# Performance work log

Measured on AMD Instinct MI355X. Metric: run time of the kernel, lower is better.

The kernel has to match this reference:

```python
import jax, jax.numpy as jnp
import numpy as np

# ---- problem constants (match init_kwargs) ----
LAM = 1.0; MU = 1.0; D0 = 1.0; NMIN = 1.0; NMAX = 99; ALPHA = 2.0
BATCH = 2048; N_STEPS = 64; T = 1.0; HIDDEN = 128


def _U(x):
    return D0 / (x + NMIN) ** ALPHA


def _delta_n(pre_n, dt, forward, k, rng):
    # faithful numpy port of PolymerDiffusion.delta_N (jump sizes shared across batch per call)
    log_res = -np.log(rng.random(k))
    lsk = np.concatenate([[0.0], np.cumsum(log_res / LAM / 2)])
    msk = np.concatenate([[0.0], np.cumsum(log_res / MU / 2)])
    jl = int(np.searchsorted(lsk[1:], dt, side='right'))  # first j with dt < lsk[j+1]
    jm = int(np.searchsorted(msk[1:], dt, side='right'))
    if jl >= k: jl = 0  # no break -> delta stays 0
    if jm >= k: jm = 0
    eta = rng.random(pre_n.shape[0])
    if forward:
        d_up = np.where(pre_n <= NMAX - jl, jl, 0)
        d_dn = np.where(pre_n >= jm, -jm, 0)
    else:
        d_up = np.where(pre_n >= jl, jl, 0)
        d_dn = np.where(pre_n <= NMAX - jm, -jm, 0)
    return np.where(eta < 0.5, d_up, d_dn).astype(np.float64)


def _get_samples(dt, N, rng):
    B = BATCH
    X1 = np.zeros((B, N + 1)); X1[:, 0] = rng.integers(0, NMAX + 1, B)
    X2 = np.zeros((B, N + 1))
    dB = rng.standard_normal((B, N)) * np.sqrt(dt)
    for i in range(N):
        X1[:, i + 1] = X1[:, i] + _delta_n(X1[:, i], dt, True, 5, rng)
        X2[:, i + 1] = X2[:, i] + _U(X1[:, i]) * dt + dB[:, i]
    X1b = rng.integers(0, NMAX + 1, (B, N + 1)).astype(np.float64)
    X2b = np.zeros((B, N + 1))
    dBb = rng.standard_normal((B, N)) * np.sqrt(dt)
    X1b[:, N] = X1[:, N]; X2b[:, N] = X2[:, N]
    for i in range(N):
        X1b[:, N - i - 1] = X1b[:, N - i] - _delta_n(X1b[:, N - i], dt, False, 5, rng)
        X2b[:, N - i - 1] = X2b[:, N - i] - _U(X1b[:, N - i]) * dt - dBb[:, N - i - 1]
    return (np.concatenate([X1, X1b], 0), np.concatenate([X2, X2b], 0), np.concatenate([dB, dBb], 0))


def setup_inputs() -> dict:
    rng = np.random.default_rng(0)
    dt = T / N_STEPS
    n_np, s_np, dB_np = _get_samples(dt, N_STEPS, rng)
    key = jax.random.key(0)
    ks = jax.random.split(key, 4)
    def w(k, fi, fo):
        return jax.random.normal(k, (fi, fo), jnp.float32) / np.sqrt(fi).astype(np.float32)
    return {
        'W1': w(ks[0], 2, HIDDEN), 'b1': jnp.zeros(HIDDEN, jnp.float32),
        'W2': w(ks[1], HIDDEN, HIDDEN), 'b2': jnp.zeros(HIDDEN, jnp.float32),
        'W3': w(ks[2], HIDDEN, HIDDEN), 'b3': jnp.zeros(HIDDEN, jnp.float32),
        'W4': w(ks[3], HIDDEN, NMAX + 1), 'b4': jnp.zeros(NMAX + 1, jnp.float32),
        'samples_n': jnp.asarray(n_np, jnp.int32),      # [2B, N+1]
        'samples_s': jnp.asarray(s_np, jnp.float32),    # [2B, N+1]
        'samples_deltaB': jnp.asarray(dB_np, jnp.float32),  # [2B, N]
        't': jnp.float32(T),
    }


def reference(W1, b1, W2, b2, W3, b3, W4, b4, samples_n, samples_s, samples_deltaB, t):
    N = samples_deltaB.shape[1]
    dt = t / N
    out_dim = W4.shape[1]  # nmax + 1

    def u_scalar(s, tk, n):
        x = jnp.stack([s, tk])  # [2]
        h = jnp.tanh(x @ W1 + b1)
        h = jnp.tanh(h @ W2 + b2)
        h = jnp.tanh(h @ W3 + b3)
        return (h @ W4 + b4)[n]

    du = jax.grad(u_scalar, 0)
    ddu = jax.grad(du, 0)
    u_v = jax.vmap(u_scalar)
    du_v = jax.vmap(du)
    ddu_v = jax.vmap(ddu)

    B2 = samples_s.shape[0]
    tk0 = jnp.broadcast_to(t, (B2,))
    sN, nN = samples_s[:, N], samples_n[:, N]
    u = u_v(sN, tk0, nN)
    ps = du_v(sN, tk0, nN)
    pss = ddu_v(sN, tk0, nN)

    # step i uses column N-1-i and time tk = t - i*dt (tk decremented AFTER get_partial, as in source)
    dB_rev = samples_deltaB[:, ::-1].T            # [N, 2B]
    s_rev = samples_s[:, N - 1::-1].T             # [N, 2B]
    n_rev = samples_n[:, N - 1::-1].T             # [N, 2B]
    tks = t - dt * jnp.arange(N, dtype=samples_s.dtype)  # [N]

    def step(carry, xs):
        u, ps, pss = carry
        dB, s_col, n_col, tk = xs
        u = u - ps * dB - pss * dt * 0.5
        tkv = jnp.broadcast_to(tk, s_col.shape)
        ps = du_v(s_col, tkv, n_col)
        pss = ddu_v(s_col, tkv, n_col)
        return (u, ps, pss), None

    (u, _, _), _ = jax.lax.scan(step, (u, ps, pss), (dB_rev, s_rev, n_rev, tks))

    beta = 1e6
    s0 = samples_s[:, 0]
    u0 = jnp.sqrt(beta / (2 * jnp.pi)) * jnp.exp(-beta * s0 ** 2 / 2) / out_dim
    return (u[:, None], u0[:, None])
```

## Files before the change

kernel.cpp:

```cpp
#include <hip/hip_runtime.h>
#include <hip/hip_fp16.h>
#include <math.h>

#define HIDDEN 128
#define NSTEP  64
#define BATCH2 4096
#define OUTD   100

typedef __attribute__((ext_vector_type(8))) _Float16 f16x8;
typedef __attribute__((ext_vector_type(4))) float    f32x4;

static __device__ __forceinline__ f32x4 mfma32(f16x8 a, f16x8 b, f32x4 c) {
    return __builtin_amdgcn_mfma_f32_16x16x32_f16(a, b, c, 0, 0, 0);
}
static __device__ __forceinline__ unsigned h2u(__half2 h) {
    return __builtin_bit_cast(unsigned, h);
}
static __device__ __forceinline__ __half2 u2h(unsigned u) {
    return __builtin_bit_cast(__half2, u);
}
static __device__ __forceinline__ f16x8 frag8(__half2 a, __half2 b, __half2 c, __half2 d) {
    uint4 p = { h2u(a), h2u(b), h2u(c), h2u(d) };
    return __builtin_bit_cast(f16x8, p);
}
static __device__ __forceinline__ f16x8 catu2(uint2 lo, uint2 hi) {
    uint4 p = { lo.x, lo.y, hi.x, hi.y };
    return __builtin_bit_cast(f16x8, p);
}

static __device__ __forceinline__ void load_lds16(const void* g, void* l) {
    __builtin_amdgcn_global_load_lds(
        (const __attribute__((address_space(1))) void*)g,
        (__attribute__((address_space(3))) void*)l, 16, 0, 0);
}

static __device__ __forceinline__ void tanh_chain_h2(
    __half2 z, __half2 zd, __half2 zdd,
    __half2& a, __half2& ad, __half2& add)
{
    const __half2 one = __float2half2_rn(1.0f);
    const __half2 two = __float2half2_rn(2.0f);
    __half2 e = h2exp(__hadd2(z, z));
    __half2 w = __hmul2(two, h2rcp(__hadd2(e, one)));
    a  = __hsub2(one, w);
    __half2 g = __hmul2(w, __hsub2(two, w));
    ad = __hmul2(g, zd);
    __half2 p = __hmul2(a, zd);
    __half2 u = __hadd2(p, p);
    add = __hsub2(__hmul2(g, zdd), __hmul2(u, ad));
}

__global__ __launch_bounds__(256) void setup_kernel(
    const float* __restrict__ W2, const float* __restrict__ W3,
    const float* __restrict__ W4,
    const float* __restrict__ b2, const float* __restrict__ b3,
    const float* __restrict__ samples_s,
    __half* __restrict__ wbf, float* __restrict__ out)
{
    int t = blockIdx.x * blockDim.x + threadIdx.x;
    {
        int l = t >> 14;
        int f = t & 16383;
        int row = f >> 7;
        int m   = f & 127;
        float v = (l ? W3 : W2)[f];
        int c, q, i;
        if (l == 0) {
            c = row >> 5; q = (row >> 3) & 3; i = row & 7;
        } else {
            c = row >> 5;
            int rem = row & 31;
            q = (rem >> 2) & 3;
            i = ((rem >> 4) << 2) | (rem & 3);
        }
        int pos = (l << 14) + ((((m >> 4) << 2) + c) << 9)
                + ((16 * q + (m & 15)) << 3) + i;
        wbf[pos] = __float2half(v);
    }
    if (t < OUTD * HIDDEN) {
        int h = t / OUTD, n = t - h * OUTD;
        wbf[32768 + n * HIDDEN + h] = __float2half(W4[t]);
    }
    if (t < 256) {
        const float* bp = (t < 128) ? b2 : b3;
        wbf[45568 + t] = __float2half(bp[t & 127]);
    }
    if (t < BATCH2) {
        out[t] = 0.0f;
        float s0 = samples_s[t * (NSTEP + 1)];
        out[BATCH2 + t] = 3.9894228040143267f * expf(-500000.0f * s0 * s0);
    }
}

__global__ __launch_bounds__(256, 4) void eval_kernel(
    const float* __restrict__ W1, const float* __restrict__ b1,
    const float* __restrict__ b4,
    const __half* __restrict__ wbf,
    const int*   __restrict__ samples_n,
    const float* __restrict__ samples_s,
    const float* __restrict__ samples_dB,
    const float* __restrict__ tptr,
    float* __restrict__ out)
{
    __shared__ __align__(16) short  ldsW[HIDDEN * HIDDEN];
    __shared__ __align__(16) __half ldsB[256];

    const int tid  = threadIdx.x;
    const int w    = tid >> 6;
    const int lane = tid & 63;
    const int m16  = lane & 15;
    const int q    = lane >> 4;
    const int b    = blockIdx.x;

    {
        const short* g2 = (const short*)wbf;
        #pragma unroll
        for (int it = 0; it < 8; ++it) {
            int idx = w * 8 + it;
            load_lds16(g2 + idx * 512 + lane * 8, ldsW + idx * 512);
        }
    }
    if (tid < 128) {
        ((unsigned*)ldsB)[tid] = ((const unsigned*)(wbf + 45568))[tid];
    }

    const float t  = tptr[0];
    const float dt = t / (float)NSTEP;
    const int   j  = 16 * w + m16;
    const int   c  = NSTEP - j;
    const float s  = samples_s[b * (NSTEP + 1) + c];
    const int   n  = samples_n[b * (NSTEP + 1) + c];
    const float dB = samples_dB[b * NSTEP + (NSTEP - 1 - j)];
    const float tk = (j == 0) ? t : t - dt * (float)(j - 1);

    f16x8 B1v[4], B1d[4], B1dd[4];
    const __half2 zero2 = __float2half2_rn(0.0f);
    #pragma unroll
    for (int ck = 0; ck < 4; ++ck) {
        const int h0 = 32 * ck + 8 * q;
        float4 wa0 = *(const float4*)(W1 + h0);
        float4 wa1 = *(const float4*)(W1 + h0 + 4);
        float4 wb0 = *(const float4*)(W1 + HIDDEN + h0);
        float4 wb1 = *(const float4*)(W1 + HIDDEN + h0 + 4);
        float4 bb0 = *(const float4*)(b1 + h0);
        float4 bb1 = *(const float4*)(b1 + h0 + 4);
        __half2 a[4], ad[4], add[4];
        {
            __half2 z  = __floats2half2_rn(fmaf(wa0.x, s, fmaf(wb0.x, tk, bb0.x)),
                                           fmaf(wa0.y, s, fmaf(wb0.y, tk, bb0.y)));
            tanh_chain_h2(z, __floats2half2_rn(wa0.x, wa0.y), zero2, a[0], ad[0], add[0]);
            z  = __floats2half2_rn(fmaf(wa0.z, s, fmaf(wb0.z, tk, bb0.z)),
                                   fmaf(wa0.w, s, fmaf(wb0.w, tk, bb0.w)));
            tanh_chain_h2(z, __floats2half2_rn(wa0.z, wa0.w), zero2, a[1], ad[1], add[1]);
            z  = __floats2half2_rn(fmaf(wa1.x, s, fmaf(wb1.x, tk, bb1.x)),
                                   fmaf(wa1.y, s, fmaf(wb1.y, tk, bb1.y)));
            tanh_chain_h2(z, __floats2half2_rn(wa1.x, wa1.y), zero2, a[2], ad[2], add[2]);
            z  = __floats2half2_rn(fmaf(wa1.z, s, fmaf(wb1.z, tk, bb1.z)),
                                   fmaf(wa1.w, s, fmaf(wb1.w, tk, bb1.w)));
            tanh_chain_h2(z, __floats2half2_rn(wa1.z, wa1.w), zero2, a[3], ad[3], add[3]);
        }
        B1v[ck]  = frag8(a[0],  a[1],  a[2],  a[3]);
        B1d[ck]  = frag8(ad[0], ad[1], ad[2], ad[3]);
        B1dd[ck] = frag8(add[0], add[1], add[2], add[3]);
    }

    __syncthreads();

    uint2 Nv[8], Nd[8], Ndd[8];
    #pragma unroll
    for (int mt = 0; mt < 8; ++mt) {
        f32x4 aV = {0.f,0.f,0.f,0.f}, aD = {0.f,0.f,0.f,0.f}, aDD = {0.f,0.f,0.f,0.f};
        #pragma unroll
        for (int ck = 0; ck < 4; ++ck) {
            f16x8 aw = *(const f16x8*)(ldsW + ((mt * 4 + ck) << 9) + (lane << 3));
            aV  = mfma32(aw, B1v[ck],  aV );
            aD  = mfma32(aw, B1d[ck],  aD );
            aDD = mfma32(aw, B1dd[ck], aDD);
        }
        uint2 bh = *(const uint2*)(ldsB + 16 * mt + 4 * q);
        __half2 z0 = __hadd2(__floats2half2_rn(aV[0], aV[1]), u2h(bh.x));
        __half2 z1 = __hadd2(__floats2half2_rn(aV[2], aV[3]), u2h(bh.y));
        __half2 a0, ad0, add0, a1, ad1, add1;
        tanh_chain_h2(z0, __floats2half2_rn(aD[0], aD[1]),
                      __floats2half2_rn(aDD[0], aDD[1]), a0, ad0, add0);
        tanh_chain_h2(z1, __floats2half2_rn(aD[2], aD[3]),
                      __floats2half2_rn(aDD[2], aDD[3]), a1, ad1, add1);
        Nv[mt]  = (uint2){ h2u(a0),  h2u(a1)  };
        Nd[mt]  = (uint2){ h2u(ad0), h2u(ad1) };
        Ndd[mt] = (uint2){ h2u(add0), h2u(add1) };
    }

    __syncthreads();

    {
        const short* g3 = (const short*)(wbf + HIDDEN * HIDDEN);
        #pragma unroll
        for (int it = 0; it < 8; ++it) {
            int idx = w * 8 + it;
            load_lds16(g3 + idx * 512 + lane * 8, ldsW + idx * 512);
        }
    }

    f16x8 B2v[4], B2d[4], B2dd[4];
    #pragma unroll
    for (int ck = 0; ck < 4; ++ck) {
        B2v[ck]  = catu2(Nv[2*ck],  Nv[2*ck+1]);
        B2d[ck]  = catu2(Nd[2*ck],  Nd[2*ck+1]);
        B2dd[ck] = catu2(Ndd[2*ck], Ndd[2*ck+1]);
    }
    __syncthreads();

    const __half* __restrict__ w4t = wbf + 2 * HIDDEN * HIDDEN;
    __half2 accV = zero2, accD = zero2, accDD = zero2;
    #pragma unroll
    for (int mt = 0; mt < 8; ++mt) {
        f32x4 aV = {0.f,0.f,0.f,0.f}, aD = {0.f,0.f,0.f,0.f}, aDD = {0.f,0.f,0.f,0.f};
        #pragma unroll
        for (int ck = 0; ck < 4; ++ck) {
            f16x8 aw = *(const f16x8*)(ldsW + ((mt * 4 + ck) << 9) + (lane << 3));
            aV  = mfma32(aw, B2v[ck],  aV );
            aD  = mfma32(aw, B2d[ck],  aD );
            aDD = mfma32(aw, B2dd[ck], aDD);
        }
        const int h0 = 16 * mt + 4 * q;
        uint2 w4u = *(const uint2*)(w4t + n * HIDDEN + h0);
        __half2 w4lo = u2h(w4u.x), w4hi = u2h(w4u.y);
        uint2 bh = *(const uint2*)(ldsB + 128 + h0);
        __half2 z0 = __hadd2(__floats2half2_rn(aV[0], aV[1]), u2h(bh.x));
        __half2 z1 = __hadd2(__floats2half2_rn(aV[2], aV[3]), u2h(bh.y));
        __half2 a0, ad0, add0, a1, ad1, add1;
        tanh_chain_h2(z0, __floats2half2_rn(aD[0], aD[1]),
                      __floats2half2_rn(aDD[0], aDD[1]), a0, ad0, add0);
        tanh_chain_h2(z1, __floats2half2_rn(aD[2], aD[3]),
                      __floats2half2_rn(aDD[2], aDD[3]), a1, ad1, add1);
        accV  = __hfma2(a0,  w4lo, accV );  accV  = __hfma2(a1,  w4hi, accV );
        accD  = __hfma2(ad0, w4lo, accD );  accD  = __hfma2(ad1, w4hi, accD );
        accDD = __hfma2(add0, w4lo, accDD); accDD = __hfma2(add1, w4hi, accDD);
    }
    float sv  = __low2float(accV)  + __high2float(accV);
    float sd  = __low2float(accD)  + __high2float(accD);
    float sdd = __low2float(accDD) + __high2float(accDD);

    sd  += __shfl_xor(sd,  16, 64);  sd  += __shfl_xor(sd,  32, 64);
    sdd += __shfl_xor(sdd, 16, 64);  sdd += __shfl_xor(sdd, 32, 64);
    sv  += __shfl_xor(sv,  16, 64);  sv  += __shfl_xor(sv,  32, 64);

    float contrib = -(sd * dB + sdd * dt * 0.5f);
    if (j == 0) contrib += sv + b4[n];

    contrib += __shfl_xor(contrib, 1, 64);
    contrib += __shfl_xor(contrib, 2, 64);
    contrib += __shfl_xor(contrib, 4, 64);
    contrib += __shfl_xor(contrib, 8, 64);
    if (lane == 0) atomicAdd(&out[b], contrib);
}

extern "C" void kernel_launch(void* const* d_in, const int* in_sizes, int n_in,
                              void* d_out, int out_size, void* d_ws, size_t ws_size,
                              hipStream_t stream) {
    const float* W1 = (const float*)d_in[0];
    const float* b1 = (const float*)d_in[1];
    const float* W2 = (const float*)d_in[2];
    const float* b2 = (const float*)d_in[3];
    const float* W3 = (const float*)d_in[4];
    const float* b3 = (const float*)d_in[5];
    const float* W4 = (const float*)d_in[6];
    const float* b4 = (const float*)d_in[7];
    const int*   sn  = (const int*)d_in[8];
    const float* ss  = (const float*)d_in[9];
    const float* sdB = (const float*)d_in[10];
    const float* t   = (const float*)d_in[11];
    float* out = (float*)d_out;
    __half* wbf = (__half*)d_ws;

    setup_kernel<<<(2 * HIDDEN * HIDDEN) / 256, 256, 0, stream>>>(
        W2, W3, W4, b2, b3, ss, wbf, out);
    eval_kernel<<<BATCH2, 256, 0, stream>>>(
        W1, b1, b4, wbf, sn, ss, sdB, t, out);
}
```

Baseline: 148.6 us.

## Process two batch samples per block to amortize LDS weight loads

Each eval block now handles two batch rows, so the W2/W3 weight tiles staged into LDS are reused across two samples and half as many blocks run. The per-block partial sums are combined through a small LDS buffer and written directly, replacing the atomicAdd. Output zeroing and the u0 computation move from the setup kernel into the eval kernel. Register pressure roughly doubles for activation fragments, so the occupancy hint drops from 4 to 3 waves per SIMD, which risks lower latency hiding.

```diff
diff --git a/kernel.cpp b/kernel.cpp
--- a/kernel.cpp
+++ b/kernel.cpp
@@ -54,8 +54,7 @@
     const float* __restrict__ W2, const float* __restrict__ W3,
     const float* __restrict__ W4,
     const float* __restrict__ b2, const float* __restrict__ b3,
-    const float* __restrict__ samples_s,
-    __half* __restrict__ wbf, float* __restrict__ out)
+    __half* __restrict__ wbf)
 {
     int t = blockIdx.x * blockDim.x + threadIdx.x;
     {
@@ -85,14 +84,9 @@
         const float* bp = (t < 128) ? b2 : b3;
         wbf[45568 + t] = __float2half(bp[t & 127]);
     }
-    if (t < BATCH2) {
-        out[t] = 0.0f;
-        float s0 = samples_s[t * (NSTEP + 1)];
-        out[BATCH2 + t] = 3.9894228040143267f * expf(-500000.0f * s0 * s0);
-    }
-}
-
-__global__ __launch_bounds__(256, 4) void eval_kernel(
+}
+
+__global__ __launch_bounds__(256, 3) void eval_kernel(
     const float* __restrict__ W1, const float* __restrict__ b1,
     const float* __restrict__ b4,
     const __half* __restrict__ wbf,
@@ -104,13 +98,14 @@
 {
     __shared__ __align__(16) short  ldsW[HIDDEN * HIDDEN];
     __shared__ __align__(16) __half ldsB[256];
+    __shared__ float ldsR[2][4];
 
     const int tid  = threadIdx.x;
     const int w    = tid >> 6;
     const int lane = tid & 63;
     const int m16  = lane & 15;
     const int q    = lane >> 4;
-    const int b    = blockIdx.x;
+    const int b0   = blockIdx.x * 2;
 
     {
         const short* g2 = (const short*)wbf;
@@ -128,12 +123,17 @@
     const float dt = t / (float)NSTEP;
     const int   j  = 16 * w + m16;
     const int   c  = NSTEP - j;
-    const float s  = samples_s[b * (NSTEP + 1) + c];
-    const int   n  = samples_n[b * (NSTEP + 1) + c];
-    const float dB = samples_dB[b * NSTEP + (NSTEP - 1 - j)];
     const float tk = (j == 0) ? t : t - dt * (float)(j - 1);
-
-    f16x8 B1v[4], B1d[4], B1dd[4];
+    float sS[2]; int nn[2]; float dBs[2];
+    #pragma unroll
+    for (int p = 0; p < 2; ++p) {
+        int bb = b0 + p;
+        sS[p]  = samples_s[bb * (NSTEP + 1) + c];
+        nn[p]  = samples_n[bb * (NSTEP + 1) + c];
+        dBs[p] = samples_dB[bb * NSTEP + (NSTEP - 1 - j)];
+    }
+
+    f16x8 B1v[2][4], B1d[2][4], B1dd[2][4];
     const __half2 zero2 = __float2half2_rn(0.0f);
     #pragma unroll
     for (int ck = 0; ck < 4; ++ck) {
@@ -144,50 +144,55 @@
         float4 wb1 = *(const float4*)(W1 + HIDDEN + h0 + 4);
         float4 bb0 = *(const float4*)(b1 + h0);
         float4 bb1 = *(const float4*)(b1 + h0 + 4);
-        __half2 a[4], ad[4], add[4];
-        {
-            __half2 z  = __floats2half2_rn(fmaf(wa0.x, s, fmaf(wb0.x, tk, bb0.x)),
-                                           fmaf(wa0.y, s, fmaf(wb0.y, tk, bb0.y)));
+        #pragma unroll
+        for (int p = 0; p < 2; ++p) {
+            float s = sS[p];
+            __half2 a[4], ad[4], add[4];
+            __half2 z = __floats2half2_rn(fmaf(wa0.x, s, fmaf(wb0.x, tk, bb0.x)),
+                                          fmaf(wa0.y, s, fmaf(wb0.y, tk, bb0.y)));
             tanh_chain_h2(z, __floats2half2_rn(wa0.x, wa0.y), zero2, a[0], ad[0], add[0]);
-            z  = __floats2half2_rn(fmaf(wa0.z, s, fmaf(wb0.z, tk, bb0.z)),
-                                   fmaf(wa0.w, s, fmaf(wb0.w, tk, bb0.w)));
+            z = __floats2half2_rn(fmaf(wa0.z, s, fmaf(wb0.z, tk, bb0.z)),
+                                  fmaf(wa0.w, s, fmaf(wb0.w, tk, bb0.w)));
             tanh_chain_h2(z, __floats2half2_rn(wa0.z, wa0.w), zero2, a[1], ad[1], add[1]);
-            z  = __floats2half2_rn(fmaf(wa1.x, s, fmaf(wb1.x, tk, bb1.x)),
-                                   fmaf(wa1.y, s, fmaf(wb1.y, tk, bb1.y)));
+            z = __floats2half2_rn(fmaf(wa1.x, s, fmaf(wb1.x, tk, bb1.x)),
+                                  fmaf(wa1.y, s, fmaf(wb1.y, tk, bb1.y)));
             tanh_chain_h2(z, __floats2half2_rn(wa1.x, wa1.y), zero2, a[2], ad[2], add[2]);
-            z  = __floats2half2_rn(fmaf(wa1.z, s, fmaf(wb1.z, tk, bb1.z)),
-                                   fmaf(wa1.w, s, fmaf(wb1.w, tk, bb1.w)));
+            z = __floats2half2_rn(fmaf(wa1.z, s, fmaf(wb1.z, tk, bb1.z)),
+                                  fmaf(wa1.w, s, fmaf(wb1.w, tk, bb1.w)));
             tanh_chain_h2(z, __floats2half2_rn(wa1.z, wa1.w), zero2, a[3], ad[3], add[3]);
-        }
-        B1v[ck]  = frag8(a[0],  a[1],  a[2],  a[3]);
-        B1d[ck]  = frag8(ad[0], ad[1], ad[2], ad[3]);
-        B1dd[ck] = frag8(add[0], add[1], add[2], add[3]);
-    }
-
-    __syncthreads();
-
-    uint2 Nv[8], Nd[8], Ndd[8];
-    #pragma unroll
-    for (int mt = 0; mt < 8; ++mt) {
-        f32x4 aV = {0.f,0.f,0.f,0.f}, aD = {0.f,0.f,0.f,0.f}, aDD = {0.f,0.f,0.f,0.f};
-        #pragma unroll
-        for (int ck = 0; ck < 4; ++ck) {
-            f16x8 aw = *(const f16x8*)(ldsW + ((mt * 4 + ck) << 9) + (lane << 3));
-            aV  = mfma32(aw, B1v[ck],  aV );
-            aD  = mfma32(aw, B1d[ck],  aD );
-            aDD = mfma32(aw, B1dd[ck], aDD);
-        }
-        uint2 bh = *(const uint2*)(ldsB + 16 * mt + 4 * q);
-        __half2 z0 = __hadd2(__floats2half2_rn(aV[0], aV[1]), u2h(bh.x));
-        __half2 z1 = __hadd2(__floats2half2_rn(aV[2], aV[3]), u2h(bh.y));
-        __half2 a0, ad0, add0, a1, ad1, add1;
-        tanh_chain_h2(z0, __floats2half2_rn(aD[0], aD[1]),
-                      __floats2half2_rn(aDD[0], aDD[1]), a0, ad0, add0);
-        tanh_chain_h2(z1, __floats2half2_rn(aD[2], aD[3]),
-                      __floats2half2_rn(aDD[2], aDD[3]), a1, ad1, add1);
-        Nv[mt]  = (uint2){ h2u(a0),  h2u(a1)  };
-        Nd[mt]  = (uint2){ h2u(ad0), h2u(ad1) };
-        Ndd[mt] = (uint2){ h2u(add0), h2u(add1) };
+            B1v[p][ck]  = frag8(a[0],  a[1],  a[2],  a[3]);
+            B1d[p][ck]  = frag8(ad[0], ad[1], ad[2], ad[3]);
+            B1dd[p][ck] = frag8(add[0], add[1], add[2], add[3]);
+        }
+    }
+
+    __syncthreads();
+
+    uint2 Nv[2][8], Nd[2][8], Ndd[2][8];
+    #pragma unroll
+    for (int p = 0; p < 2; ++p) {
+        #pragma unroll
+        for (int mt = 0; mt < 8; ++mt) {
+            f32x4 aV = {0.f,0.f,0.f,0.f}, aD = {0.f,0.f,0.f,0.f}, aDD = {0.f,0.f,0.f,0.f};
+            #pragma unroll
+            for (int ck = 0; ck < 4; ++ck) {
+                f16x8 aw = *(const f16x8*)(ldsW + ((mt * 4 + ck) << 9) + (lane << 3));
+                aV  = mfma32(aw, B1v[p][ck],  aV );
+                aD  = mfma32(aw, B1d[p][ck],  aD );
+                aDD = mfma32(aw, B1dd[p][ck], aDD);
+            }
+            uint2 bh = *(const uint2*)(ldsB + 16 * mt + 4 * q);
+            __half2 z0 = __hadd2(__floats2half2_rn(aV[0], aV[1]), u2h(bh.x));
+            __half2 z1 = __hadd2(__floats2half2_rn(aV[2], aV[3]), u2h(bh.y));
+            __half2 a0, ad0, add0, a1, ad1, add1;
+            tanh_chain_h2(z0, __floats2half2_rn(aD[0], aD[1]),
+                          __floats2half2_rn(aDD[0], aDD[1]), a0, ad0, add0);
+            tanh_chain_h2(z1, __floats2half2_rn(aD[2], aD[3]),
+                          __floats2half2_rn(aDD[2], aDD[3]), a1, ad1, add1);
+            Nv[p][mt]  = (uint2){ h2u(a0),  h2u(a1)  };
+            Nd[p][mt]  = (uint2){ h2u(ad0), h2u(ad1) };
+            Ndd[p][mt] = (uint2){ h2u(add0), h2u(add1) };
+        }
     }
 
     __syncthreads();
@@ -200,59 +205,64 @@
             load_lds16(g3 + idx * 512 + lane * 8, ldsW + idx * 512);
         }
     }
-
-    f16x8 B2v[4], B2d[4], B2dd[4];
-    #pragma unroll
-    for (int ck = 0; ck < 4; ++ck) {
-        B2v[ck]  = catu2(Nv[2*ck],  Nv[2*ck+1]);
-        B2d[ck]  = catu2(Nd[2*ck],  Nd[2*ck+1]);
-        B2dd[ck] = catu2(Ndd[2*ck], Ndd[2*ck+1]);
-    }
     __syncthreads();
 
     const __half* __restrict__ w4t = wbf + 2 * HIDDEN * HIDDEN;
-    __half2 accV = zero2, accD = zero2, accDD = zero2;
-    #pragma unroll
-    for (int mt = 0; mt < 8; ++mt) {
-        f32x4 aV = {0.f,0.f,0.f,0.f}, aD = {0.f,0.f,0.f,0.f}, aDD = {0.f,0.f,0.f,0.f};
-        #pragma unroll
-        for (int ck = 0; ck < 4; ++ck) {
-            f16x8 aw = *(const f16x8*)(ldsW + ((mt * 4 + ck) << 9) + (lane << 3));
-            aV  = mfma32(aw, B2v[ck],  aV );
-            aD  = mfma32(aw, B2d[ck],  aD );
-            aDD = mfma32(aw, B2dd[ck], aDD);
-        }
-        const int h0 = 16 * mt + 4 * q;
-        uint2 w4u = *(const uint2*)(w4t + n * HIDDEN + h0);
-        __half2 w4lo = u2h(w4u.x), w4hi = u2h(w4u.y);
-        uint2 bh = *(const uint2*)(ldsB + 128 + h0);
-        __half2 z0 = __hadd2(__floats2half2_rn(aV[0], aV[1]), u2h(bh.x));
-        __half2 z1 = __hadd2(__floats2half2_rn(aV[2], aV[3]), u2h(bh.y));
-        __half2 a0, ad0, add0, a1, ad1, add1;
-        tanh_chain_h2(z0, __floats2half2_rn(aD[0], aD[1]),
-                      __floats2half2_rn(aDD[0], aDD[1]), a0, ad0, add0);
-        tanh_chain_h2(z1, __floats2half2_rn(aD[2], aD[3]),
-                      __floats2half2_rn(aDD[2], aDD[3]), a1, ad1, add1);
-        accV  = __hfma2(a0,  w4lo, accV );  accV  = __hfma2(a1,  w4hi, accV );
-        accD  = __hfma2(ad0, w4lo, accD );  accD  = __hfma2(ad1, w4hi, accD );
-        accDD = __hfma2(add0, w4lo, accDD); accDD = __hfma2(add1, w4hi, accDD);
-    }
-    float sv  = __low2float(accV)  + __high2float(accV);
-    float sd  = __low2float(accD)  + __high2float(accD);
-    float sdd = __low2float(accDD) + __high2float(accDD);
-
-    sd  += __shfl_xor(sd,  16, 64);  sd  += __shfl_xor(sd,  32, 64);
-    sdd += __shfl_xor(sdd, 16, 64);  sdd += __shfl_xor(sdd, 32, 64);
-    sv  += __shfl_xor(sv,  16, 64);  sv  += __shfl_xor(sv,  32, 64);
-
-    float contrib = -(sd * dB + sdd * dt * 0.5f);
-    if (j == 0) contrib += sv + b4[n];
-
-    contrib += __shfl_xor(contrib, 1, 64);
-    contrib += __shfl_xor(contrib, 2, 64);
-    contrib += __shfl_xor(contrib, 4, 64);
-    contrib += __shfl_xor(contrib, 8, 64);
-    if (lane == 0) atomicAdd(&out[b], contrib);
+    float contrib[2];
+    #pragma unroll
+    for (int p = 0; p < 2; ++p) {
+        __half2 accV = zero2, accD = zero2, accDD = zero2;
+        #pragma unroll
+        for (int mt = 0; mt < 8; ++mt) {
+            f32x4 aV = {0.f,0.f,0.f,0.f}, aD = {0.f,0.f,0.f,0.f}, aDD = {0.f,0.f,0.f,0.f};
+            #pragma unroll
+            for (int ck = 0; ck < 4; ++ck) {
+                f16x8 aw = *(const f16x8*)(ldsW + ((mt * 4 + ck) << 9) + (lane << 3));
+                aV  = mfma32(aw, catu2(Nv[p][2*ck],  Nv[p][2*ck+1]),  aV );
+                aD  = mfma32(aw, catu2(Nd[p][2*ck],  Nd[p][2*ck+1]),  aD );
+                aDD = mfma32(aw, catu2(Ndd[p][2*ck], Ndd[p][2*ck+1]), aDD);
+            }
+            const int h0 = 16 * mt + 4 * q;
+            uint2 w4u = *(const uint2*)(w4t + nn[p] * HIDDEN + h0);
+            __half2 w4lo = u2h(w4u.x), w4hi = u2h(w4u.y);
+            uint2 bh = *(const uint2*)(ldsB + 128 + h0);
+            __half2 z0 = __hadd2(__floats2half2_rn(aV[0], aV[1]), u2h(bh.x));
+            __half2 z1 = __hadd2(__floats2half2_rn(aV[2], aV[3]), u2h(bh.y));
+            __half2 a0, ad0, add0, a1, ad1, add1;
+            tanh_chain_h2(z0, __floats2half2_rn(aD[0], aD[1]),
+                          __floats2half2_rn(aDD[0], aDD[1]), a0, ad0, add0);
+            tanh_chain_h2(z1, __floats2half2_rn(aD[2], aD[3]),
+                          __floats2half2_rn(aDD[2], aDD[3]), a1, ad1, add1);
+            accV  = __hfma2(a0,  w4lo, accV );  accV  = __hfma2(a1,  w4hi, accV );
+            accD  = __hfma2(ad0, w4lo, accD );  accD  = __hfma2(ad1, w4hi, accD );
+            accDD = __hfma2(add0, w4lo, accDD); accDD = __hfma2(add1, w4hi, accDD);
+        }
+        float sv  = __low2float(accV)  + __high2float(accV);
+        float sd  = __low2float(accD)  + __high2float(accD);
+        float sdd = __low2float(accDD) + __high2float(accDD);
+        sd  += __shfl_xor(sd,  16, 64);  sd  += __shfl_xor(sd,  32, 64);
+        sdd += __shfl_xor(sdd, 16, 64);  sdd += __shfl_xor(sdd, 32, 64);
+        sv  += __shfl_xor(sv,  16, 64);  sv  += __shfl_xor(sv,  32, 64);
+        float cb = -(sd * dBs[p] + sdd * dt * 0.5f);
+        if (j == 0) cb += sv + b4[nn[p]];
+        cb += __shfl_xor(cb, 1, 64);
+        cb += __shfl_xor(cb, 2, 64);
+        cb += __shfl_xor(cb, 4, 64);
+        cb += __shfl_xor(cb, 8, 64);
+        contrib[p] = cb;
+    }
+    if (lane == 0) {
+        ldsR[0][w] = contrib[0];
+        ldsR[1][w] = contrib[1];
+    }
+    __syncthreads();
+
+    if (tid < 2) {
+        float u = ldsR[tid][0] + ldsR[tid][1] + ldsR[tid][2] + ldsR[tid][3];
+        out[b0 + tid] = u;
+        float s0 = samples_s[(b0 + tid) * (NSTEP + 1)];
+        out[BATCH2 + b0 + tid] = 3.9894228040143267f * expf(-500000.0f * s0 * s0);
+    }
 }
 
 extern "C" void kernel_launch(void* const* d_in, const int* in_sizes, int n_in,
@@ -274,7 +284,7 @@
     __half* wbf = (__half*)d_ws;
 
     setup_kernel<<<(2 * HIDDEN * HIDDEN) / 256, 256, 0, stream>>>(
-        W2, W3, W4, b2, b3, ss, wbf, out);
-    eval_kernel<<<BATCH2, 256, 0, stream>>>(
+        W2, W3, W4, b2, b3, wbf);
+    eval_kernel<<<BATCH2 / 2, 256, 0, stream>>>(
         W1, b1, b4, wbf, sn, ss, sdB, t, out);
 }
```

Result: slower. 243.0 us (+63.6%).

## Read MLP weights straight from global memory instead of staging in LDS

Applied to the files above, without the earlier changes.

Removes the 32 KB LDS staging of W2/W3 and biases, along with the three block barriers, and has each wave load its MFMA A-fragments directly from global memory (L1/L2 cached). Dropping LDS use can raise occupancy and removes the synchronisation points. The cost is repeated global/L2 traffic for the same weights across waves and blocks, with load latency now exposed at each MFMA. It also limits the value-accumulator work to wave 0.

```diff
diff --git a/kernel.cpp b/kernel.cpp
--- a/kernel.cpp
+++ b/kernel.cpp
@@ -26,12 +26,6 @@
 static __device__ __forceinline__ f16x8 catu2(uint2 lo, uint2 hi) {
     uint4 p = { lo.x, lo.y, hi.x, hi.y };
     return __builtin_bit_cast(f16x8, p);
-}
-
-static __device__ __forceinline__ void load_lds16(const void* g, void* l) {
-    __builtin_amdgcn_global_load_lds(
-        (const __attribute__((address_space(1))) void*)g,
-        (__attribute__((address_space(3))) void*)l, 16, 0, 0);
 }
 
 static __device__ __forceinline__ void tanh_chain_h2(
@@ -102,27 +96,12 @@
     const float* __restrict__ tptr,
     float* __restrict__ out)
 {
-    __shared__ __align__(16) short  ldsW[HIDDEN * HIDDEN];
-    __shared__ __align__(16) __half ldsB[256];
-
     const int tid  = threadIdx.x;
     const int w    = tid >> 6;
     const int lane = tid & 63;
     const int m16  = lane & 15;
     const int q    = lane >> 4;
     const int b    = blockIdx.x;
-
-    {
-        const short* g2 = (const short*)wbf;
-        #pragma unroll
-        for (int it = 0; it < 8; ++it) {
-            int idx = w * 8 + it;
-            load_lds16(g2 + idx * 512 + lane * 8, ldsW + idx * 512);
-        }
-    }
-    if (tid < 128) {
-        ((unsigned*)ldsB)[tid] = ((const unsigned*)(wbf + 45568))[tid];
-    }
 
     const float t  = tptr[0];
     const float dt = t / (float)NSTEP;
@@ -132,6 +111,10 @@
     const int   n  = samples_n[b * (NSTEP + 1) + c];
     const float dB = samples_dB[b * NSTEP + (NSTEP - 1 - j)];
     const float tk = (j == 0) ? t : t - dt * (float)(j - 1);
+
+    const short* gW2 = (const short*)wbf + (lane << 3);
+    const short* gW3 = (const short*)(wbf + HIDDEN * HIDDEN) + (lane << 3);
+    const __half* bia = wbf + 45568;
 
     f16x8 B1v[4], B1d[4], B1dd[4];
     const __half2 zero2 = __float2half2_rn(0.0f);
@@ -164,20 +147,18 @@
         B1dd[ck] = frag8(add[0], add[1], add[2], add[3]);
     }
 
-    __syncthreads();
-
     uint2 Nv[8], Nd[8], Ndd[8];
     #pragma unroll
     for (int mt = 0; mt < 8; ++mt) {
         f32x4 aV = {0.f,0.f,0.f,0.f}, aD = {0.f,0.f,0.f,0.f}, aDD = {0.f,0.f,0.f,0.f};
         #pragma unroll
         for (int ck = 0; ck < 4; ++ck) {
-            f16x8 aw = *(const f16x8*)(ldsW + ((mt * 4 + ck) << 9) + (lane << 3));
+            f16x8 aw = *(const f16x8*)(gW2 + ((mt * 4 + ck) << 9));
             aV  = mfma32(aw, B1v[ck],  aV );
             aD  = mfma32(aw, B1d[ck],  aD );
             aDD = mfma32(aw, B1dd[ck], aDD);
         }
-        uint2 bh = *(const uint2*)(ldsB + 16 * mt + 4 * q);
+        uint2 bh = *(const uint2*)(bia + 16 * mt + 4 * q);
         __half2 z0 = __hadd2(__floats2half2_rn(aV[0], aV[1]), u2h(bh.x));
         __half2 z1 = __hadd2(__floats2half2_rn(aV[2], aV[3]), u2h(bh.y));
         __half2 a0, ad0, add0, a1, ad1, add1;
@@ -190,26 +171,6 @@
         Ndd[mt] = (uint2){ h2u(add0), h2u(add1) };
     }
 
-    __syncthreads();
-
-    {
-        const short* g3 = (const short*)(wbf + HIDDEN * HIDDEN);
-        #pragma unroll
-        for (int it = 0; it < 8; ++it) {
-            int idx = w * 8 + it;
-            load_lds16(g3 + idx * 512 + lane * 8, ldsW + idx * 512);
-        }
-    }
-
-    f16x8 B2v[4], B2d[4], B2dd[4];
-    #pragma unroll
-    for (int ck = 0; ck < 4; ++ck) {
-        B2v[ck]  = catu2(Nv[2*ck],  Nv[2*ck+1]);
-        B2d[ck]  = catu2(Nd[2*ck],  Nd[2*ck+1]);
-        B2dd[ck] = catu2(Ndd[2*ck], Ndd[2*ck+1]);
-    }
-    __syncthreads();
-
     const __half* __restrict__ w4t = wbf + 2 * HIDDEN * HIDDEN;
     __half2 accV = zero2, accD = zero2, accDD = zero2;
     #pragma unroll
@@ -217,15 +178,15 @@
         f32x4 aV = {0.f,0.f,0.f,0.f}, aD = {0.f,0.f,0.f,0.f}, aDD = {0.f,0.f,0.f,0.f};
         #pragma unroll
         for (int ck = 0; ck < 4; ++ck) {
-            f16x8 aw = *(const f16x8*)(ldsW + ((mt * 4 + ck) << 9) + (lane << 3));
-            aV  = mfma32(aw, B2v[ck],  aV );
-            aD  = mfma32(aw, B2d[ck],  aD );
-            aDD = mfma32(aw, B2dd[ck], aDD);
+            f16x8 aw = *(const f16x8*)(gW3 + ((mt * 4 + ck) << 9));
+            aV  = mfma32(aw, catu2(Nv[2*ck],  Nv[2*ck+1]),  aV );
+            aD  = mfma32(aw, catu2(Nd[2*ck],  Nd[2*ck+1]),  aD );
+            aDD = mfma32(aw, catu2(Ndd[2*ck], Ndd[2*ck+1]), aDD);
         }
         const int h0 = 16 * mt + 4 * q;
         uint2 w4u = *(const uint2*)(w4t + n * HIDDEN + h0);
         __half2 w4lo = u2h(w4u.x), w4hi = u2h(w4u.y);
-        uint2 bh = *(const uint2*)(ldsB + 128 + h0);
+        uint2 bh = *(const uint2*)(bia + 128 + h0);
         __half2 z0 = __hadd2(__floats2half2_rn(aV[0], aV[1]), u2h(bh.x));
         __half2 z1 = __hadd2(__floats2half2_rn(aV[2], aV[3]), u2h(bh.y));
         __half2 a0, ad0, add0, a1, ad1, add1;
@@ -233,20 +194,24 @@
                       __floats2half2_rn(aDD[0], aDD[1]), a0, ad0, add0);
         tanh_chain_h2(z1, __floats2half2_rn(aD[2], aD[3]),
                       __floats2half2_rn(aDD[2], aDD[3]), a1, ad1, add1);
-        accV  = __hfma2(a0,  w4lo, accV );  accV  = __hfma2(a1,  w4hi, accV );
         accD  = __hfma2(ad0, w4lo, accD );  accD  = __hfma2(ad1, w4hi, accD );
         accDD = __hfma2(add0, w4lo, accDD); accDD = __hfma2(add1, w4hi, accDD);
-    }
-    float sv  = __low2float(accV)  + __high2float(accV);
+        if (w == 0) {
+            accV = __hfma2(a0, w4lo, accV);  accV = __hfma2(a1, w4hi, accV);
+        }
+    }
     float sd  = __low2float(accD)  + __high2float(accD);
     float sdd = __low2float(accDD) + __high2float(accDD);
 
     sd  += __shfl_xor(sd,  16, 64);  sd  += __shfl_xor(sd,  32, 64);
     sdd += __shfl_xor(sdd, 16, 64);  sdd += __shfl_xor(sdd, 32, 64);
-    sv  += __shfl_xor(sv,  16, 64);  sv  += __shfl_xor(sv,  32, 64);
 
     float contrib = -(sd * dB + sdd * dt * 0.5f);
-    if (j == 0) contrib += sv + b4[n];
+    if (w == 0) {
+        float sv = __low2float(accV) + __high2float(accV);
+        sv += __shfl_xor(sv, 16, 64);  sv += __shfl_xor(sv, 32, 64);
+        if (j == 0) contrib += sv + b4[n];
+    }
 
     contrib += __shfl_xor(contrib, 1, 64);
     contrib += __shfl_xor(contrib, 2, 64);
```

Result: slower. 154.4 us (+3.9%).

## Process two samples per block and replace atomics with an LDS reduction

Applied to the files above, without the earlier changes.

Each 512-thread block now handles two batch samples, so every staged W2/W3 tile in LDS is shared by twice the work and each wave loads half as many chunks. The per-sample atomicAdd is replaced by an LDS reduction followed by a plain store. The output zeroing and u0 computation move from the setup kernel into the eval kernel. The value-path accumulation now runs only in the wave that needs it, and the B-fragment concatenation is inlined into the MFMA loop to relieve register pressure. In exchange, launch bounds of 512 threads and 8 blocks may limit registers and occupancy.

```diff
diff --git a/kernel.cpp b/kernel.cpp
--- a/kernel.cpp
+++ b/kernel.cpp
@@ -54,8 +54,7 @@
     const float* __restrict__ W2, const float* __restrict__ W3,
     const float* __restrict__ W4,
     const float* __restrict__ b2, const float* __restrict__ b3,
-    const float* __restrict__ samples_s,
-    __half* __restrict__ wbf, float* __restrict__ out)
+    __half* __restrict__ wbf)
 {
     int t = blockIdx.x * blockDim.x + threadIdx.x;
     {
@@ -85,14 +84,9 @@
         const float* bp = (t < 128) ? b2 : b3;
         wbf[45568 + t] = __float2half(bp[t & 127]);
     }
-    if (t < BATCH2) {
-        out[t] = 0.0f;
-        float s0 = samples_s[t * (NSTEP + 1)];
-        out[BATCH2 + t] = 3.9894228040143267f * expf(-500000.0f * s0 * s0);
-    }
-}
-
-__global__ __launch_bounds__(256, 4) void eval_kernel(
+}
+
+__global__ __launch_bounds__(512, 8) void eval_kernel(
     const float* __restrict__ W1, const float* __restrict__ b1,
     const float* __restrict__ b4,
     const __half* __restrict__ wbf,
@@ -104,19 +98,22 @@
 {
     __shared__ __align__(16) short  ldsW[HIDDEN * HIDDEN];
     __shared__ __align__(16) __half ldsB[256];
+    __shared__ float ldsR[2][4];
 
     const int tid  = threadIdx.x;
     const int w    = tid >> 6;
+    const int p    = w >> 2;
+    const int jw   = w & 3;
     const int lane = tid & 63;
     const int m16  = lane & 15;
     const int q    = lane >> 4;
-    const int b    = blockIdx.x;
+    const int b    = blockIdx.x * 2 + p;
 
     {
         const short* g2 = (const short*)wbf;
         #pragma unroll
-        for (int it = 0; it < 8; ++it) {
-            int idx = w * 8 + it;
+        for (int it = 0; it < 4; ++it) {
+            int idx = w * 4 + it;
             load_lds16(g2 + idx * 512 + lane * 8, ldsW + idx * 512);
         }
     }
@@ -126,7 +123,7 @@
 
     const float t  = tptr[0];
     const float dt = t / (float)NSTEP;
-    const int   j  = 16 * w + m16;
+    const int   j  = 16 * jw + m16;
     const int   c  = NSTEP - j;
     const float s  = samples_s[b * (NSTEP + 1) + c];
     const int   n  = samples_n[b * (NSTEP + 1) + c];
@@ -195,18 +192,10 @@
     {
         const short* g3 = (const short*)(wbf + HIDDEN * HIDDEN);
         #pragma unroll
-        for (int it = 0; it < 8; ++it) {
-            int idx = w * 8 + it;
+        for (int it = 0; it < 4; ++it) {
+            int idx = w * 4 + it;
             load_lds16(g3 + idx * 512 + lane * 8, ldsW + idx * 512);
         }
-    }
-
-    f16x8 B2v[4], B2d[4], B2dd[4];
-    #pragma unroll
-    for (int ck = 0; ck < 4; ++ck) {
-        B2v[ck]  = catu2(Nv[2*ck],  Nv[2*ck+1]);
-        B2d[ck]  = catu2(Nd[2*ck],  Nd[2*ck+1]);
-        B2dd[ck] = catu2(Ndd[2*ck], Ndd[2*ck+1]);
     }
     __syncthreads();
 
@@ -218,9 +207,9 @@
         #pragma unroll
         for (int ck = 0; ck < 4; ++ck) {
             f16x8 aw = *(const f16x8*)(ldsW + ((mt * 4 + ck) << 9) + (lane << 3));
-            aV  = mfma32(aw, B2v[ck],  aV );
-            aD  = mfma32(aw, B2d[ck],  aD );
-            aDD = mfma32(aw, B2dd[ck], aDD);
+            aV  = mfma32(aw, catu2(Nv[2*ck],  Nv[2*ck+1]),  aV );
+            aD  = mfma32(aw, catu2(Nd[2*ck],  Nd[2*ck+1]),  aD );
+            aDD = mfma32(aw, catu2(Ndd[2*ck], Ndd[2*ck+1]), aDD);
         }
         const int h0 = 16 * mt + 4 * q;
         uint2 w4u = *(const uint2*)(w4t + n * HIDDEN + h0);
@@ -233,26 +222,38 @@
                       __floats2half2_rn(aDD[0], aDD[1]), a0, ad0, add0);
         tanh_chain_h2(z1, __floats2half2_rn(aD[2], aD[3]),
                       __floats2half2_rn(aDD[2], aDD[3]), a1, ad1, add1);
-        accV  = __hfma2(a0,  w4lo, accV );  accV  = __hfma2(a1,  w4hi, accV );
         accD  = __hfma2(ad0, w4lo, accD );  accD  = __hfma2(ad1, w4hi, accD );
         accDD = __hfma2(add0, w4lo, accDD); accDD = __hfma2(add1, w4hi, accDD);
-    }
-    float sv  = __low2float(accV)  + __high2float(accV);
+        if (jw == 0) {
+            accV = __hfma2(a0, w4lo, accV);  accV = __hfma2(a1, w4hi, accV);
+        }
+    }
     float sd  = __low2float(accD)  + __high2float(accD);
     float sdd = __low2float(accDD) + __high2float(accDD);
 
     sd  += __shfl_xor(sd,  16, 64);  sd  += __shfl_xor(sd,  32, 64);
     sdd += __shfl_xor(sdd, 16, 64);  sdd += __shfl_xor(sdd, 32, 64);
-    sv  += __shfl_xor(sv,  16, 64);  sv  += __shfl_xor(sv,  32, 64);
 
     float contrib = -(sd * dB + sdd * dt * 0.5f);
-    if (j == 0) contrib += sv + b4[n];
+    if (jw == 0) {
+        float sv = __low2float(accV) + __high2float(accV);
+        sv += __shfl_xor(sv, 16, 64);  sv += __shfl_xor(sv, 32, 64);
+        if (j == 0) contrib += sv + b4[n];
+    }
 
     contrib += __shfl_xor(contrib, 1, 64);
     contrib += __shfl_xor(contrib, 2, 64);
     contrib += __shfl_xor(contrib, 4, 64);
     contrib += __shfl_xor(contrib, 8, 64);
-    if (lane == 0) atomicAdd(&out[b], contrib);
+    if (lane == 0) ldsR[p][jw] = contrib;
+    __syncthreads();
+
+    if (tid < 2) {
+        int bb = blockIdx.x * 2 + tid;
+        out[bb] = ldsR[tid][0] + ldsR[tid][1] + ldsR[tid][2] + ldsR[tid][3];
+        float s0 = samples_s[bb * (NSTEP + 1)];
+        out[BATCH2 + bb] = 3.9894228040143267f * expf(-500000.0f * s0 * s0);
+    }
 }
 
 extern "C" void kernel_launch(void* const* d_in, const int* in_sizes, int n_in,
@@ -274,7 +275,7 @@
     __half* wbf = (__half*)d_ws;
 
     setup_kernel<<<(2 * HIDDEN * HIDDEN) / 256, 256, 0, stream>>>(
-        W2, W3, W4, b2, b3, ss, wbf, out);
-    eval_kernel<<<BATCH2, 256, 0, stream>>>(
+        W2, W3, W4, b2, b3, wbf);
+    eval_kernel<<<BATCH2 / 2, 512, 0, stream>>>(
         W1, b1, b4, wbf, sn, ss, sdB, t, out);
 }
```

After: 359.4 us. 142% more time.
